# Performance work log

Hardware: AMD Instinct MI355X
Metric: run time of the kernel (lower is better)

## Reference

```python
import jax, jax.numpy as jnp
import numpy as np

D = 768
EXPAND = 4
D_INNER = EXPAND * D
G = 32
EPS = 1e-5


def setup_inputs() -> dict:
    key = jax.random.key(0)
    ks = jax.random.split(key, 10)
    B, T = 16, G * G
    s = lambda fan_in: 1.0 / np.sqrt(fan_in)
    return {
        "x": jax.random.normal(ks[0], (B, T, D), dtype=jnp.float32),
        "norm_w": jnp.ones((D,), dtype=jnp.float32),
        "w_proj": jax.random.normal(ks[1], (D_INNER, D), dtype=jnp.float32) * s(D),
        "w_gate": jax.random.normal(ks[2], (D_INNER, D), dtype=jnp.float32) * s(D),
        "conv_w": jax.random.normal(ks[3], (D_INNER, 1, 3, 3), dtype=jnp.float32) * s(9),
        "conv_b": jax.random.normal(ks[4], (D_INNER,), dtype=jnp.float32) * 0.01,
        "w_out": jax.random.normal(ks[5], (D, D_INNER), dtype=jnp.float32) * s(D_INNER),
        "w_k": jax.random.normal(ks[6], (D, D), dtype=jnp.float32) * s(D),
        "w_v": jax.random.normal(ks[7], (D, D), dtype=jnp.float32) * s(D),
        "log_alpha": jnp.array(0.0, dtype=jnp.float32),  # log(memory_alpha=1.0)
    }


def _rmsnorm(x, w):
    ms = jnp.mean(jnp.square(x.astype(jnp.float32)), axis=-1, keepdims=True)
    return x * jax.lax.rsqrt(ms + EPS).astype(x.dtype) * w


def reference(x, norm_w, w_proj, w_gate, conv_w, conv_b, w_out, w_k, w_v, log_alpha):
    B, T, _ = x.shape
    h = _rmsnorm(x, norm_w)                                   # [B,T,D]
    val = jnp.einsum("btd,ed->bte", h, w_proj)                # [B,T,dI]
    val = val.transpose(0, 2, 1).reshape(B, D_INNER, G, G)    # [B,dI,G,G]
    val = jax.lax.conv_general_dilated(
        val, conv_w, window_strides=(1, 1), padding=((1, 1), (1, 1)),
        dimension_numbers=("NCHW", "OIHW", "NCHW"),
        feature_group_count=D_INNER,
    ) + conv_b[None, :, None, None]
    val = jax.nn.silu(val)
    val = val.reshape(B, D_INNER, T).transpose(0, 2, 1)       # [B,T,dI]
    gated = val * jax.nn.silu(jnp.einsum("btd,ed->bte", h, w_gate))
    out = jnp.einsum("bte,de->btd", gated, w_out)             # [B,T,D]
    K = jnp.einsum("btd,ed->bte", h, w_k)                     # [B,T,D]
    V = jnp.einsum("btd,ed->bte", out, w_v)                   # [B,T,D]
    W = jnp.einsum("btd,bte->bde", K, V) / T                  # [B,D,D]
    read = jnp.einsum("btd,bde->bte", K, W)                   # [B,T,D]
    out = out + jnp.exp(log_alpha) * read
    return x + out
```

## Files before the change

kernel.cpp:

```cpp
#include <hip/hip_runtime.h>
#include <hip/hip_bf16.h>
#include <cstdint>
#include <cstddef>

typedef unsigned short u16;
typedef __attribute__((ext_vector_type(8))) __bf16 bf16x8;
typedef __attribute__((ext_vector_type(4))) float f32x4;
typedef __attribute__((ext_vector_type(8))) unsigned short us8;

#define NDM 768
#define NDI 3072
#define NTT 1024
#define NBB 16
#define NM (NBB*NTT)

__device__ __forceinline__ u16 f2bf(float f) {
  unsigned u = __builtin_bit_cast(unsigned, f);
  u += 0x7fffu + ((u >> 16) & 1u);
  return (u16)(u >> 16);
}
__device__ __forceinline__ float bf2f(u16 b) {
  return __builtin_bit_cast(float, ((unsigned)b) << 16);
}
__device__ __forceinline__ float silu_f(float v) {
  return v * (1.0f / (1.0f + __expf(-v)));
}
__device__ __forceinline__ void gload16(const u16* g, u16* l) {
  __builtin_amdgcn_global_load_lds((const __attribute__((address_space(1))) void*)g,
                                   (__attribute__((address_space(3))) void*)l, 16, 0, 0);
}

__global__ __launch_bounds__(256)
void k_f32_to_bf16(const float* __restrict__ in, u16* __restrict__ out, int n4) {
  const int i = blockIdx.x * 256 + threadIdx.x;
  if (i < n4) {
    float4 v = ((const float4*)in)[i];
    ushort4 o;
    o.x = f2bf(v.x); o.y = f2bf(v.y); o.z = f2bf(v.z); o.w = f2bf(v.w);
    ((ushort4*)out)[i] = o;
  }
}

__global__ __launch_bounds__(256)
void k_convw_t(const float* __restrict__ cw, u16* __restrict__ wTb) {
  const int e = blockIdx.x * 256 + threadIdx.x;
  if (e < NDI) {
#pragma unroll
    for (int t = 0; t < 9; t++) wTb[t * NDI + e] = f2bf(cw[e * 9 + t]);
  }
}

__global__ __launch_bounds__(256)
void k_rmsnorm(const float* __restrict__ x, const float* __restrict__ w, u16* __restrict__ h) {
  const int row  = blockIdx.x * 4 + (threadIdx.x >> 6);
  const int lane = threadIdx.x & 63;
  const float4* xr = (const float4*)(x + (size_t)row * NDM);
  float4 a = xr[lane], b = xr[lane + 64], c = xr[lane + 128];
  float ss = a.x*a.x + a.y*a.y + a.z*a.z + a.w*a.w
           + b.x*b.x + b.y*b.y + b.z*b.z + b.w*b.w
           + c.x*c.x + c.y*c.y + c.z*c.z + c.w*c.w;
#pragma unroll
  for (int off = 32; off > 0; off >>= 1) ss += __shfl_xor(ss, off);
  const float r = rsqrtf(ss * (1.0f / NDM) + 1e-5f);
  const float4* wr = (const float4*)w;
  float4 wa = wr[lane], wb = wr[lane + 64], wc = wr[lane + 128];
  ushort4 oa, ob, oc;
  oa.x = f2bf(a.x * r * wa.x); oa.y = f2bf(a.y * r * wa.y);
  oa.z = f2bf(a.z * r * wa.z); oa.w = f2bf(a.w * r * wa.w);
  ob.x = f2bf(b.x * r * wb.x); ob.y = f2bf(b.y * r * wb.y);
  ob.z = f2bf(b.z * r * wb.z); ob.w = f2bf(b.w * r * wb.w);
  oc.x = f2bf(c.x * r * wc.x); oc.y = f2bf(c.y * r * wc.y);
  oc.z = f2bf(c.z * r * wc.z); oc.w = f2bf(c.w * r * wc.w);
  ushort4* hr = (ushort4*)(h + (size_t)row * NDM);
  hr[lane] = oa; hr[lane + 64] = ob; hr[lane + 128] = oc;
}

template <int MODE>
__global__ __launch_bounds__(256)
void k_gemm_nt(const u16* __restrict__ A, const u16* __restrict__ B,
               void* __restrict__ C0, void* __restrict__ C1,
               const float* __restrict__ X, const float* __restrict__ scalep,
               int N, int Kd, int nTiles,
               long sAb, long sBb, long sCb, int mPerBatchB, long sBm) {
  __shared__ u16 As[128 * 32];
  __shared__ u16 Bs[128 * 32];
  const int bz = blockIdx.z;
  A += (size_t)bz * sAb;
  B += (size_t)bz * sBb;

  const int nwg = gridDim.x;
  const int id = blockIdx.x;
  const int sid = ((nwg & 7) == 0) ? ((id & 7) * (nwg >> 3) + (id >> 3)) : id;
  const int mt = sid / nTiles, nt = sid - mt * nTiles;
  const int m0 = mt * 128, n0 = nt * 128;
  if (mPerBatchB > 0) B += (size_t)(m0 / mPerBatchB) * sBm;

  const int lane = threadIdx.x & 63, wid = threadIdx.x >> 6;
  const int wm = wid >> 1, wn = wid & 1;

  f32x4 zero = {0.f, 0.f, 0.f, 0.f};
  f32x4 acc[4][4];
#pragma unroll
  for (int m = 0; m < 4; m++)
#pragma unroll
    for (int n = 0; n < 4; n++) acc[m][n] = zero;

  const u16* Ag = A + (size_t)(m0 + wid * 32 + (lane >> 2)) * Kd + (lane & 3) * 8;
  const u16* Bg = B + (size_t)(n0 + wid * 32 + (lane >> 2)) * Kd + (lane & 3) * 8;
  u16* AsW = &As[(wid * 32) * 32];
  u16* BsW = &Bs[(wid * 32) * 32];
  const int rowSkip = 16 * Kd;
  const int fr = lane & 15, fko = (lane >> 4) * 8;

  for (int kt = 0; kt < Kd; kt += 32) {
    gload16(Ag, AsW);
    gload16(Ag + rowSkip, AsW + 16 * 32);
    gload16(Bg, BsW);
    gload16(Bg + rowSkip, BsW + 16 * 32);
    Ag += 32; Bg += 32;
    __syncthreads();
    bf16x8 af[4], bfr[4];
#pragma unroll
    for (int m = 0; m < 4; m++)
      af[m] = *(const bf16x8*)&As[(wm * 64 + m * 16 + fr) * 32 + fko];
#pragma unroll
    for (int n = 0; n < 4; n++)
      bfr[n] = *(const bf16x8*)&Bs[(wn * 64 + n * 16 + fr) * 32 + fko];
#pragma unroll
    for (int m = 0; m < 4; m++)
#pragma unroll
      for (int n = 0; n < 4; n++)
        acc[m][n] = __builtin_amdgcn_mfma_f32_16x16x32_bf16(af[m], bfr[n], acc[m][n], 0, 0, 0);
    __syncthreads();
  }

  float sc = 1.0f;
  if (MODE == 2) sc = __expf(scalep[0]) * (1.0f / 1024.0f);
  const size_t cb = (size_t)bz * sCb;
#pragma unroll
  for (int m = 0; m < 4; m++) {
#pragma unroll
    for (int n = 0; n < 4; n++) {
      const int col = n0 + wn * 64 + n * 16 + (lane & 15);
      const int rb  = m0 + wm * 64 + m * 16 + ((lane >> 4) << 2);
#pragma unroll
      for (int q = 0; q < 4; q++) {
        const float v = acc[m][n][q];
        if (MODE == 0) {
          ((u16*)C0)[cb + (size_t)(rb + q) * N + col] = f2bf(v);
        } else if (MODE == 2) {
          ((u16*)C0)[cb + (size_t)(rb + q) * N + col] = f2bf(v * sc);
        } else if (MODE == 3) {
          const size_t idx = (size_t)(rb + q) * N + col;
          ((float*)C0)[idx] = X[idx] + bf2f(((const u16*)C1)[idx]) + v;
        } else {
          if (n0 < 3072) ((u16*)C0)[(size_t)(rb + q) * 3072 + col] = f2bf(v);
          else           ((u16*)C1)[(size_t)(rb + q) * 3072 + (col - 3072)] = f2bf(silu_f(v));
        }
      }
    }
  }
}

__global__ __launch_bounds__(384)
void k_conv_gate(const u16* __restrict__ val, u16* __restrict__ gate,
                 const u16* __restrict__ wTb, const float* __restrict__ bias) {
  const int tid = threadIdx.x;
  const int m = blockIdx.x * 2 + (tid >= 192);
  const int e0 = (tid % 192) * 16;
  const int j = m & 31, i = (m >> 5) & 31;
  float acc[16];
  {
    const float4* bp = (const float4*)(bias + e0);
    float4 b0 = bp[0], b1 = bp[1], b2 = bp[2], b3 = bp[3];
    acc[0]=b0.x; acc[1]=b0.y; acc[2]=b0.z; acc[3]=b0.w;
    acc[4]=b1.x; acc[5]=b1.y; acc[6]=b1.z; acc[7]=b1.w;
    acc[8]=b2.x; acc[9]=b2.y; acc[10]=b2.z; acc[11]=b2.w;
    acc[12]=b3.x; acc[13]=b3.y; acc[14]=b3.z; acc[15]=b3.w;
  }
  const u16* vb = val + (size_t)m * NDI + e0;
#pragma unroll
  for (int di = -1; di <= 1; di++) {
    if ((unsigned)(i + di) >= 32u) continue;
#pragma unroll
    for (int dj = -1; dj <= 1; dj++) {
      if ((unsigned)(j + dj) >= 32u) continue;
      const u16* vp = vb + (ptrdiff_t)(di * 32 + dj) * NDI;
      us8 v0 = *(const us8*)vp, v1 = *(const us8*)(vp + 8);
      const u16* wp = wTb + ((di + 1) * 3 + (dj + 1)) * NDI + e0;
      us8 w0 = *(const us8*)wp, w1 = *(const us8*)(wp + 8);
#pragma unroll
      for (int q = 0; q < 8; q++) acc[q]     += bf2f(v0[q]) * bf2f(w0[q]);
#pragma unroll
      for (int q = 0; q < 8; q++) acc[8 + q] += bf2f(v1[q]) * bf2f(w1[q]);
    }
  }
  u16* gp = gate + (size_t)m * NDI + e0;
  us8 g0 = *(const us8*)gp, g1 = *(const us8*)(gp + 8);
  us8 o0, o1;
#pragma unroll
  for (int q = 0; q < 8; q++) o0[q] = f2bf(silu_f(acc[q]) * bf2f(g0[q]));
#pragma unroll
  for (int q = 0; q < 8; q++) o1[q] = f2bf(silu_f(acc[8 + q]) * bf2f(g1[q]));
  *(us8*)gp = o0;
  *(us8*)(gp + 8) = o1;
}

__global__ __launch_bounds__(256)
void k_transpose(const u16* __restrict__ in, u16* __restrict__ out) {
  __shared__ u16 tile[64][65];
  const int d0 = blockIdx.x * 64, t0 = blockIdx.y * 64, b = blockIdx.z;
  const int lx = threadIdx.x & 15, ly = threadIdx.x >> 4;
  const u16* ip = in + ((size_t)b * NTT + t0) * NDM + d0;
#pragma unroll
  for (int p = 0; p < 4; p++) {
    const int r = ly + p * 16;
    ushort4 v = *(const ushort4*)(ip + (size_t)r * NDM + lx * 4);
    tile[r][lx * 4 + 0] = v.x; tile[r][lx * 4 + 1] = v.y;
    tile[r][lx * 4 + 2] = v.z; tile[r][lx * 4 + 3] = v.w;
  }
  __syncthreads();
  u16* op = out + ((size_t)b * NDM + d0) * NTT + t0;
#pragma unroll
  for (int p = 0; p < 4; p++) {
    const int r = ly + p * 16;
    ushort4 v;
    v.x = tile[lx * 4 + 0][r]; v.y = tile[lx * 4 + 1][r];
    v.z = tile[lx * 4 + 2][r]; v.w = tile[lx * 4 + 3][r];
    *(ushort4*)(op + (size_t)r * NTT + lx * 4) = v;
  }
}

extern "C" void kernel_launch(void* const* d_in, const int* in_sizes, int n_in,
                              void* d_out, int out_size, void* d_ws, size_t ws_size,
                              hipStream_t stream) {
  const float* x      = (const float*)d_in[0];
  const float* norm_w = (const float*)d_in[1];
  const float* w_proj = (const float*)d_in[2];
  const float* w_gate = (const float*)d_in[3];
  const float* conv_w = (const float*)d_in[4];
  const float* conv_b = (const float*)d_in[5];
  const float* w_out  = (const float*)d_in[6];
  const float* w_k    = (const float*)d_in[7];
  const float* w_v    = (const float*)d_in[8];
  const float* lalpha = (const float*)d_in[9];

  char* ob = (char*)d_out;
  u16* h    = (u16*)(ob);
  u16* wcat = (u16*)(ob + 25165824);
  u16* wob  = (u16*)(ob + 34603008);
  u16* wkb  = (u16*)(ob + 39321600);
  u16* wvb  = (u16*)(ob + 40501248);
  u16* wTb  = (u16*)(ob + 41680896);

  char* ws = (char*)d_ws;
  u16* valp  = (u16*)(ws);
  u16* gateb = (u16*)(ws + 100663296);
  u16* outb  = (u16*)(ws);
  u16* Kbf   = (u16*)(ws + 25165824);
  u16* Vbf   = (u16*)(ws + 50331648);
  u16* Kt    = (u16*)(ws + 100663296);
  u16* Vt    = (u16*)(ws + 125829120);
  u16* Wt    = (u16*)(ws + 150994944);

  k_f32_to_bf16<<<2304, 256, 0, stream>>>(w_proj, wcat,           589824);
  k_f32_to_bf16<<<2304, 256, 0, stream>>>(w_gate, wcat + 2359296, 589824);
  k_f32_to_bf16<<<2304, 256, 0, stream>>>(w_out,  wob, 589824);
  k_f32_to_bf16<<<576,  256, 0, stream>>>(w_k,    wkb, 147456);
  k_f32_to_bf16<<<576,  256, 0, stream>>>(w_v,    wvb, 147456);
  k_convw_t<<<12, 256, 0, stream>>>(conv_w, wTb);

  k_rmsnorm<<<4096, 256, 0, stream>>>(x, norm_w, h);

  k_gemm_nt<5><<<6144, 256, 0, stream>>>(h, wcat, valp, gateb, nullptr, nullptr,
                                         6144, NDM, 48, 0, 0, 0, 0, 0);
  k_conv_gate<<<8192, 384, 0, stream>>>(valp, gateb, wTb, conv_b);

  k_gemm_nt<0><<<768, 256, 0, stream>>>(gateb, wob, outb, nullptr, nullptr, nullptr,
                                        NDM, NDI, 6, 0, 0, 0, 0, 0);
  k_gemm_nt<0><<<768, 256, 0, stream>>>(h, wkb, Kbf, nullptr, nullptr, nullptr,
                                        NDM, NDM, 6, 0, 0, 0, 0, 0);
  k_gemm_nt<0><<<768, 256, 0, stream>>>(outb, wvb, Vbf, nullptr, nullptr, nullptr,
                                        NDM, NDM, 6, 0, 0, 0, 0, 0);
  k_transpose<<<dim3(12, 16, 16), 256, 0, stream>>>(Kbf, Kt);
  k_transpose<<<dim3(12, 16, 16), 256, 0, stream>>>(Vbf, Vt);

  k_gemm_nt<2><<<dim3(36, 1, 16), 256, 0, stream>>>(Vt, Kt, Wt, nullptr, nullptr, lalpha,
                                                    NDM, NTT, 6,
                                                    (long)NDM * NTT, (long)NDM * NTT,
                                                    (long)NDM * NDM, 0, 0);
  k_gemm_nt<3><<<768, 256, 0, stream>>>(Kbf, Wt, d_out, outb, x, nullptr,
                                        NDM, NDM, 6, 0, 0, 0,
                                        NTT, (long)NDM * NDM);
}
```

Measured before the change: 749.5 us.

## Replace GEMM with 256x256-tile double-buffered swizzled-LDS MFMA kernel

Replaces the 128x128, single-buffered BK=32 GEMM with a 512-thread kernel. It computes 256x256 output tiles, uses BK=64 and double-buffers LDS with explicit vmcnt waits so global loads overlap MFMA work. LDS rows use an XOR swizzle to avoid bank conflicts, and each wave holds an 8x4 fragment block for more operand reuse. The cost is fewer workgroups for the 768-wide GEMMs (192 or 144 blocks on a large GPU) and 128KB of LDS per block, which limits occupancy.

```diff
diff --git a/kernel.cpp b/kernel.cpp
--- a/kernel.cpp
+++ b/kernel.cpp
@@ -75,87 +75,114 @@
   hr[lane] = oa; hr[lane + 64] = ob; hr[lane + 128] = oc;
 }
 
+__device__ __forceinline__ void stage8k(const u16* Asrc, const u16* Bsrc, u16* smem,
+                                        int cur, int wid, int Kd) {
+  u16* Ad = smem + cur * 16384 + wid * 512;
+  u16* Bd = smem + 32768 + cur * 16384 + wid * 512;
+  const size_t blk = (size_t)64 * Kd;
+#pragma unroll
+  for (int i = 0; i < 4; i++) {
+    gload16(Asrc + i * blk, Ad + i * 4096);
+    gload16(Bsrc + i * blk, Bd + i * 4096);
+  }
+}
+
 template <int MODE>
-__global__ __launch_bounds__(256)
-void k_gemm_nt(const u16* __restrict__ A, const u16* __restrict__ B,
-               void* __restrict__ C0, void* __restrict__ C1,
-               const float* __restrict__ X, const float* __restrict__ scalep,
-               int N, int Kd, int nTiles,
-               long sAb, long sBb, long sCb, int mPerBatchB, long sBm) {
-  __shared__ u16 As[128 * 32];
-  __shared__ u16 Bs[128 * 32];
+__global__ __launch_bounds__(512, 2)
+void k_g8(const u16* __restrict__ A, const u16* __restrict__ B,
+          void* __restrict__ C0, void* __restrict__ C1,
+          const float* __restrict__ X, const float* __restrict__ scalep,
+          int N, int Kd, int nkt, int nTiles,
+          long sAb, long sBb, long sCb, int mPerBatchB, long sBm) {
+  __shared__ u16 smem[65536];
   const int bz = blockIdx.z;
   A += (size_t)bz * sAb;
   B += (size_t)bz * sBb;
-
   const int nwg = gridDim.x;
   const int id = blockIdx.x;
   const int sid = ((nwg & 7) == 0) ? ((id & 7) * (nwg >> 3) + (id >> 3)) : id;
-  const int mt = sid / nTiles, nt = sid - mt * nTiles;
-  const int m0 = mt * 128, n0 = nt * 128;
+  const int mt = sid / nTiles, ntile = sid - mt * nTiles;
+  const int m0 = mt * 256, n0 = ntile * 256;
   if (mPerBatchB > 0) B += (size_t)(m0 / mPerBatchB) * sBm;
 
-  const int lane = threadIdx.x & 63, wid = threadIdx.x >> 6;
-  const int wm = wid >> 1, wn = wid & 1;
-
-  f32x4 zero = {0.f, 0.f, 0.f, 0.f};
-  f32x4 acc[4][4];
-#pragma unroll
-  for (int m = 0; m < 4; m++)
-#pragma unroll
-    for (int n = 0; n < 4; n++) acc[m][n] = zero;
-
-  const u16* Ag = A + (size_t)(m0 + wid * 32 + (lane >> 2)) * Kd + (lane & 3) * 8;
-  const u16* Bg = B + (size_t)(n0 + wid * 32 + (lane >> 2)) * Kd + (lane & 3) * 8;
-  u16* AsW = &As[(wid * 32) * 32];
-  u16* BsW = &Bs[(wid * 32) * 32];
-  const int rowSkip = 16 * Kd;
-  const int fr = lane & 15, fko = (lane >> 4) * 8;
-
-  for (int kt = 0; kt < Kd; kt += 32) {
-    gload16(Ag, AsW);
-    gload16(Ag + rowSkip, AsW + 16 * 32);
-    gload16(Bg, BsW);
-    gload16(Bg + rowSkip, BsW + 16 * 32);
-    Ag += 32; Bg += 32;
-    __syncthreads();
-    bf16x8 af[4], bfr[4];
-#pragma unroll
-    for (int m = 0; m < 4; m++)
-      af[m] = *(const bf16x8*)&As[(wm * 64 + m * 16 + fr) * 32 + fko];
-#pragma unroll
-    for (int n = 0; n < 4; n++)
-      bfr[n] = *(const bf16x8*)&Bs[(wn * 64 + n * 16 + fr) * 32 + fko];
-#pragma unroll
-    for (int m = 0; m < 4; m++)
-#pragma unroll
-      for (int n = 0; n < 4; n++)
-        acc[m][n] = __builtin_amdgcn_mfma_f32_16x16x32_bf16(af[m], bfr[n], acc[m][n], 0, 0, 0);
-    __syncthreads();
+  const int tid = threadIdx.x;
+  const int lane = tid & 63, wid = tid >> 6;
+  const int wm = wid >> 2, wn = wid & 3;
+  const int fr = lane & 15, l4 = lane >> 4;
+
+  const int srow = tid >> 3;
+  const int sslot = (tid & 7) ^ (srow & 7);
+  const u16* Asrc = A + (size_t)(m0 + srow) * Kd + sslot * 8;
+  const u16* Bsrc = B + (size_t)(n0 + srow) * Kd + sslot * 8;
+
+  f32x4 acc[8][4];
+#pragma unroll
+  for (int m = 0; m < 8; m++)
+#pragma unroll
+    for (int n = 0; n < 4; n++) acc[m][n] = (f32x4){0.f, 0.f, 0.f, 0.f};
+
+  stage8k(Asrc,      Bsrc,      smem, 0, wid, Kd);
+  stage8k(Asrc + 64, Bsrc + 64, smem, 1, wid, Kd);
+
+  int cur = 0;
+#pragma unroll 1
+  for (int t = 0; t < nkt; t++) {
+    if (t == nkt - 1) asm volatile("s_waitcnt vmcnt(0)" ::: "memory");
+    else              asm volatile("s_waitcnt vmcnt(8)" ::: "memory");
+    __builtin_amdgcn_s_barrier();
+
+    const u16* Abuf = smem + cur * 16384;
+    const u16* Bbuf = smem + 32768 + cur * 16384;
+
+    bf16x8 bfrag[4][2];
+#pragma unroll
+    for (int nf = 0; nf < 4; nf++) {
+      const int brow = wn * 64 + nf * 16 + fr;
+#pragma unroll
+      for (int s = 0; s < 2; s++)
+        bfrag[nf][s] = *(const bf16x8*)&Bbuf[brow * 64 + (((s << 2) + l4) ^ (brow & 7)) * 8];
+    }
+#pragma unroll
+    for (int mf = 0; mf < 8; mf++) {
+      const int arow = wm * 128 + mf * 16 + fr;
+      bf16x8 a0 = *(const bf16x8*)&Abuf[arow * 64 + ((l4)     ^ (arow & 7)) * 8];
+      bf16x8 a1 = *(const bf16x8*)&Abuf[arow * 64 + ((4 + l4) ^ (arow & 7)) * 8];
+#pragma unroll
+      for (int nf = 0; nf < 4; nf++) {
+        acc[mf][nf] = __builtin_amdgcn_mfma_f32_16x16x32_bf16(a0, bfrag[nf][0], acc[mf][nf], 0, 0, 0);
+        acc[mf][nf] = __builtin_amdgcn_mfma_f32_16x16x32_bf16(a1, bfrag[nf][1], acc[mf][nf], 0, 0, 0);
+      }
+    }
+    asm volatile("s_waitcnt lgkmcnt(0)" ::: "memory");
+    __builtin_amdgcn_s_barrier();
+    if (t < nkt - 2) stage8k(Asrc + (size_t)(t + 2) * 64, Bsrc + (size_t)(t + 2) * 64,
+                             smem, cur, wid, Kd);
+    cur ^= 1;
   }
 
   float sc = 1.0f;
   if (MODE == 2) sc = __expf(scalep[0]) * (1.0f / 1024.0f);
   const size_t cb = (size_t)bz * sCb;
 #pragma unroll
-  for (int m = 0; m < 4; m++) {
-#pragma unroll
-    for (int n = 0; n < 4; n++) {
-      const int col = n0 + wn * 64 + n * 16 + (lane & 15);
-      const int rb  = m0 + wm * 64 + m * 16 + ((lane >> 4) << 2);
+  for (int mf = 0; mf < 8; mf++) {
+#pragma unroll
+    for (int nf = 0; nf < 4; nf++) {
+      const int lc = wn * 64 + nf * 16 + fr;
+      const int rb = m0 + wm * 128 + mf * 16 + (l4 << 2);
 #pragma unroll
       for (int q = 0; q < 4; q++) {
-        const float v = acc[m][n][q];
+        float v = acc[mf][nf][q];
         if (MODE == 0) {
-          ((u16*)C0)[cb + (size_t)(rb + q) * N + col] = f2bf(v);
+          ((u16*)C0)[cb + (size_t)(rb + q) * N + n0 + lc] = f2bf(v);
         } else if (MODE == 2) {
-          ((u16*)C0)[cb + (size_t)(rb + q) * N + col] = f2bf(v * sc);
+          ((u16*)C0)[cb + (size_t)(rb + q) * N + n0 + lc] = f2bf(v * sc);
         } else if (MODE == 3) {
-          const size_t idx = (size_t)(rb + q) * N + col;
+          const size_t idx = (size_t)(rb + q) * N + n0 + lc;
           ((float*)C0)[idx] = X[idx] + bf2f(((const u16*)C1)[idx]) + v;
         } else {
-          if (n0 < 3072) ((u16*)C0)[(size_t)(rb + q) * 3072 + col] = f2bf(v);
-          else           ((u16*)C1)[(size_t)(rb + q) * 3072 + (col - 3072)] = f2bf(silu_f(v));
+          const int gc = n0 + lc;
+          if (gc < 3072) ((u16*)C0)[(size_t)(rb + q) * 3072 + gc] = f2bf(v);
+          else           ((u16*)C1)[(size_t)(rb + q) * 3072 + gc - 3072] = f2bf(silu_f(v));
         }
       }
     }
@@ -272,24 +299,24 @@
 
   k_rmsnorm<<<4096, 256, 0, stream>>>(x, norm_w, h);
 
-  k_gemm_nt<5><<<6144, 256, 0, stream>>>(h, wcat, valp, gateb, nullptr, nullptr,
-                                         6144, NDM, 48, 0, 0, 0, 0, 0);
+  k_g8<5><<<1536, 512, 0, stream>>>(h, wcat, valp, gateb, nullptr, nullptr,
+                                    3072, 768, 12, 24, 0, 0, 0, 0, 0);
   k_conv_gate<<<8192, 384, 0, stream>>>(valp, gateb, wTb, conv_b);
 
-  k_gemm_nt<0><<<768, 256, 0, stream>>>(gateb, wob, outb, nullptr, nullptr, nullptr,
-                                        NDM, NDI, 6, 0, 0, 0, 0, 0);
-  k_gemm_nt<0><<<768, 256, 0, stream>>>(h, wkb, Kbf, nullptr, nullptr, nullptr,
-                                        NDM, NDM, 6, 0, 0, 0, 0, 0);
-  k_gemm_nt<0><<<768, 256, 0, stream>>>(outb, wvb, Vbf, nullptr, nullptr, nullptr,
-                                        NDM, NDM, 6, 0, 0, 0, 0, 0);
+  k_g8<0><<<192, 512, 0, stream>>>(gateb, wob, outb, nullptr, nullptr, nullptr,
+                                   768, 3072, 48, 3, 0, 0, 0, 0, 0);
+  k_g8<0><<<192, 512, 0, stream>>>(h, wkb, Kbf, nullptr, nullptr, nullptr,
+                                   768, 768, 12, 3, 0, 0, 0, 0, 0);
+  k_g8<0><<<192, 512, 0, stream>>>(outb, wvb, Vbf, nullptr, nullptr, nullptr,
+                                   768, 768, 12, 3, 0, 0, 0, 0, 0);
   k_transpose<<<dim3(12, 16, 16), 256, 0, stream>>>(Kbf, Kt);
   k_transpose<<<dim3(12, 16, 16), 256, 0, stream>>>(Vbf, Vt);
 
-  k_gemm_nt<2><<<dim3(36, 1, 16), 256, 0, stream>>>(Vt, Kt, Wt, nullptr, nullptr, lalpha,
-                                                    NDM, NTT, 6,
-                                                    (long)NDM * NTT, (long)NDM * NTT,
-                                                    (long)NDM * NDM, 0, 0);
-  k_gemm_nt<3><<<768, 256, 0, stream>>>(Kbf, Wt, d_out, outb, x, nullptr,
-                                        NDM, NDM, 6, 0, 0, 0,
-                                        NTT, (long)NDM * NDM);
-}
+  k_g8<2><<<dim3(9, 1, 16), 512, 0, stream>>>(Vt, Kt, Wt, nullptr, nullptr, lalpha,
+                                              768, 1024, 16, 3,
+                                              (long)NDM * NTT, (long)NDM * NTT,
+                                              (long)NDM * NDM, 0, 0);
+  k_g8<3><<<192, 512, 0, stream>>>(Kbf, Wt, d_out, outb, x, nullptr,
+                                   768, 768, 12, 3, 0, 0, 0,
+                                   NTT, (long)NDM * NDM);
+}
```

After: 701.3 us. 1.07x faster.
